# Performance work log

Hardware: AMD Instinct MI355X
Metric: run time of the kernel (lower is better)

Reference implementation:

```python
import jax, jax.numpy as jnp
import numpy as np

ITERATION = 10

def setup_inputs() -> dict:
    key = jax.random.key(0)
    k1, k2, k3 = jax.random.split(key, 3)
    a_inter = jax.random.normal(k1, (8, 64, 64, 32, 32), dtype=jnp.float32)
    logits = jax.random.normal(k2, (8, 64), dtype=jnp.float32)
    W = jax.random.normal(k3, (1, 64, 64), dtype=jnp.float32)
    return {"a_inter": a_inter, "logits": logits, "W": W}


def reference(a_inter, logits, W):
    N = W.shape[1]  # num_nodes
    B = a_inter.shape[0]
    # feats: [B, N, C*H*W]
    feats = a_inter[:, :, :N, :, :].reshape(B, N, -1)
    # expand logits [B, N] -> [B, N, N] (unsqueeze(1).expand in torch)
    logits0 = jnp.broadcast_to(logits[:, None, :], (B, N, N))

    feats_norm = jnp.linalg.norm(feats, ord=2, axis=2, keepdims=True)  # [B, N, 1]
    pairwise_norm = feats_norm @ jnp.swapaxes(feats_norm, 1, 2)        # [B, N, N]
    pairwise_dot = feats @ jnp.swapaxes(feats, 1, 2)                   # [B, N, N]
    pairwise_sim = pairwise_dot / (pairwise_norm + 1e-6)
    W_sym = (W + jnp.swapaxes(W, 1, 2)) / 2.0
    pairwise_potential = pairwise_sim * W_sym                          # [B, N, N]

    unary_potential = logits0

    def body(i, l):
        probs = jnp.swapaxes(jax.nn.sigmoid(l), 1, 2)  # [B, N, N]
        # probs*pp - (1-probs)*pp == (2*probs - 1)*pp
        pp_E = jnp.sum((2.0 * probs - 1.0) * pairwise_potential, axis=2, keepdims=True)
        return unary_potential + pp_E

    logits_out = jax.lax.fori_loop(0, ITERATION, body, logits0)
    return logits_out.mean(axis=1)  # [B, N]
```

## Files before the change

### kernel.cpp

```cpp
#include <hip/hip_runtime.h>
#include <math.h>

#define BATCH 8
#define NN 64
#define DD 65536
#define CH 128
#define KC (DD / CH)
#define BK 64
#define NIT (KC / BK)
#define LSTRIDE 72

typedef float  floatx4 __attribute__((ext_vector_type(4)));
typedef __bf16 bf16x8  __attribute__((ext_vector_type(8)));

static __device__ __forceinline__ unsigned short f2bf(float f) {
    union { float f; unsigned u; } x;
    x.f = f;
    unsigned r = x.u + 0x7FFFu + ((x.u >> 16) & 1u);
    return (unsigned short)(r >> 16);
}

__global__ __launch_bounds__(256) void gram_partial_kernel(const float* __restrict__ a,
                                                           float* __restrict__ part) {
    __shared__ __align__(16) unsigned short lds[2][NN * LSTRIDE];

    const int bid = blockIdx.x;
    const int b = bid >> 7;
    const int c = bid & (CH - 1);
    const float* base = a + (size_t)b * NN * DD + (size_t)c * KC;

    const int tid  = threadIdx.x;
    const int w    = tid >> 6;
    const int lane = tid & 63;
    const int m    = lane & 15;
    const int q    = lane >> 4;

    int rowv[4], kqv[4];
    for (int sub = 0; sub < 4; ++sub) {
        int F = sub * 256 + tid;
        rowv[sub] = F >> 4;
        kqv[sub]  = F & 15;
    }

    floatx4 acc[4];
    for (int t = 0; t < 4; ++t) acc[t] = (floatx4)0.0f;

    float4 regs[4];
    for (int sub = 0; sub < 4; ++sub)
        regs[sub] = *(const float4*)(base + (size_t)rowv[sub] * DD + kqv[sub] * 4);

    for (int kt = 0; kt < NIT; ++kt) {
        unsigned short* buf = lds[kt & 1];

        for (int sub = 0; sub < 4; ++sub) {
            ushort4 h;
            h.x = f2bf(regs[sub].x);
            h.y = f2bf(regs[sub].y);
            h.z = f2bf(regs[sub].z);
            h.w = f2bf(regs[sub].w);
            *reinterpret_cast<ushort4*>(&buf[rowv[sub] * LSTRIDE + kqv[sub] * 4]) = h;
        }
        __syncthreads();

        if (kt + 1 < NIT) {
            const float* nb = base + (size_t)(kt + 1) * BK;
            for (int sub = 0; sub < 4; ++sub)
                regs[sub] = *(const float4*)(nb + (size_t)rowv[sub] * DD + kqv[sub] * 4);
        }

        for (int s = 0; s < 2; ++s) {
            int kb = s * 32 + q * 8;
            bf16x8 fr[4];
            for (int t = 0; t < 4; ++t)
                fr[t] = *reinterpret_cast<const bf16x8*>(&buf[(16 * t + m) * LSTRIDE + kb]);
            bf16x8 A = fr[w];
            for (int t = 0; t < 4; ++t)
                acc[t] = __builtin_amdgcn_mfma_f32_16x16x32_bf16(A, fr[t], acc[t], 0, 0, 0);
        }
    }

    float* pg = part + (size_t)bid * (NN * NN);
    for (int t = 0; t < 4; ++t)
        for (int r = 0; r < 4; ++r) {
            int i = 16 * w + q * 4 + r;
            int j = 16 * t + m;
            pg[i * NN + j] = acc[t][r];
        }
}

__global__ __launch_bounds__(128) void gram_reduce_kernel(const float* __restrict__ part,
                                                          float* __restrict__ gram) {
    const int gid = blockIdx.x * 128 + threadIdx.x;
    const int b   = gid >> 12;
    const int idx = gid & 4095;
    const float* p = part + (size_t)b * CH * (NN * NN) + idx;

    float s0 = 0.f, s1 = 0.f, s2 = 0.f, s3 = 0.f;
    #pragma unroll
    for (int c = 0; c < CH; c += 4) {
        s0 += p[(size_t)(c + 0) * (NN * NN)];
        s1 += p[(size_t)(c + 1) * (NN * NN)];
        s2 += p[(size_t)(c + 2) * (NN * NN)];
        s3 += p[(size_t)(c + 3) * (NN * NN)];
    }
    gram[gid] = (s0 + s1) + (s2 + s3);
}

__global__ __launch_bounds__(256) void crf_kernel(const float* __restrict__ gram,
                                                  const float* __restrict__ logits,
                                                  const float* __restrict__ Wm,
                                                  float* __restrict__ out) {
    __shared__ float pp[NN][NN + 1];
    __shared__ float E[NN];
    __shared__ float nrm[NN];
    __shared__ float part[4 * NN];

    const int b  = blockIdx.x;
    const int tid = threadIdx.x;
    const int i  = tid & 63;
    const int jq = tid >> 6;
    const float* g = gram + b * NN * NN;

    if (jq == 0) nrm[i] = sqrtf(g[i * NN + i]);
    E[i] = 0.0f;
    __syncthreads();

    const float ni = nrm[i];
    for (int jj = 0; jj < 16; ++jj) {
        int j = jq * 16 + jj;
        float wsym = 0.5f * (Wm[i * NN + j] + Wm[j * NN + i]);
        pp[i][j] = g[i * NN + j] / (ni * nrm[j] + 1e-6f) * wsym;
    }
    const float li = logits[b * NN + i];
    __syncthreads();

    for (int it = 0; it < 10; ++it) {
        float acc = 0.0f;
        for (int jj = 0; jj < 16; ++jj) {
            int j = jq * 16 + jj;
            float t = li + E[j];
            float s = 1.0f / (1.0f + expf(-t));
            acc = fmaf(2.0f * s - 1.0f, pp[i][j], acc);
        }
        part[jq * NN + i] = acc;
        __syncthreads();
        if (jq == 0)
            E[i] = part[i] + part[NN + i] + part[2 * NN + i] + part[3 * NN + i];
        __syncthreads();
    }

    if (tid < 64) {
        float s = E[tid];
        for (int off = 32; off > 0; off >>= 1) s += __shfl_down(s, off);
        float meanE = __shfl(s, 0) * (1.0f / 64.0f);
        out[b * NN + tid] = logits[b * NN + tid] + meanE;
    }
}

extern "C" void kernel_launch(void* const* d_in, const int* in_sizes, int n_in,
                              void* d_out, int out_size, void* d_ws, size_t ws_size,
                              hipStream_t stream) {
    const float* a      = (const float*)d_in[0];
    const float* logits = (const float*)d_in[1];
    const float* Wm     = (const float*)d_in[2];
    float* out  = (float*)d_out;

    float* part = (float*)d_ws;
    float* gram = part + (size_t)BATCH * CH * NN * NN;

    gram_partial_kernel<<<BATCH * CH, 256, 0, stream>>>(a, part);
    gram_reduce_kernel<<<(BATCH * NN * NN) / 128, 128, 0, stream>>>(part, gram);
    crf_kernel<<<BATCH, 256, 0, stream>>>(gram, logits, Wm, out);
}
```

Before: 261.2 us.

## Load MFMA fragments directly from global memory, dropping LDS staging

The gram partial kernel stops staging bf16 tiles through shared memory. Each lane now loads its MFMA fragments straight from global memory, converts them by truncation with a byte-permute instead of round-to-nearest, and unrolls the whole K loop without barriers. The partial output is written in a tiled 16x16 layout, and the reduce kernel's indexing is adjusted to match. This removes the LDS round trip and the __syncthreads calls. In exchange, each row is loaded redundantly by all four waves and bf16 truncation adds rounding bias.

```diff
diff --git a/kernel.cpp b/kernel.cpp
--- a/kernel.cpp
+++ b/kernel.cpp
@@ -6,28 +6,26 @@
 #define DD 65536
 #define CH 128
 #define KC (DD / CH)
-#define BK 64
-#define NIT (KC / BK)
-#define LSTRIDE 72
+#define KSTEPS (KC / 32)
 
 typedef float  floatx4 __attribute__((ext_vector_type(4)));
 typedef __bf16 bf16x8  __attribute__((ext_vector_type(8)));
 
-static __device__ __forceinline__ unsigned short f2bf(float f) {
-    union { float f; unsigned u; } x;
-    x.f = f;
-    unsigned r = x.u + 0x7FFFu + ((x.u >> 16) & 1u);
-    return (unsigned short)(r >> 16);
+static __device__ __forceinline__ bf16x8 cvt8(float4 lo, float4 hi) {
+    const unsigned sel = 0x07060302u;
+    union { unsigned u[4]; bf16x8 v; } r;
+    r.u[0] = __builtin_amdgcn_perm(__float_as_uint(lo.y), __float_as_uint(lo.x), sel);
+    r.u[1] = __builtin_amdgcn_perm(__float_as_uint(lo.w), __float_as_uint(lo.z), sel);
+    r.u[2] = __builtin_amdgcn_perm(__float_as_uint(hi.y), __float_as_uint(hi.x), sel);
+    r.u[3] = __builtin_amdgcn_perm(__float_as_uint(hi.w), __float_as_uint(hi.z), sel);
+    return r.v;
 }
 
-__global__ __launch_bounds__(256) void gram_partial_kernel(const float* __restrict__ a,
-                                                           float* __restrict__ part) {
-    __shared__ __align__(16) unsigned short lds[2][NN * LSTRIDE];
-
+__global__ __launch_bounds__(256, 4) void gram_partial_kernel(const float* __restrict__ a,
+                                                              float* __restrict__ part) {
     const int bid = blockIdx.x;
     const int b = bid >> 7;
     const int c = bid & (CH - 1);
-    const float* base = a + (size_t)b * NN * DD + (size_t)c * KC;
 
     const int tid  = threadIdx.x;
     const int w    = tid >> 6;
@@ -35,57 +33,49 @@
     const int m    = lane & 15;
     const int q    = lane >> 4;
 
-    int rowv[4], kqv[4];
-    for (int sub = 0; sub < 4; ++sub) {
-        int F = sub * 256 + tid;
-        rowv[sub] = F >> 4;
-        kqv[sub]  = F & 15;
-    }
+    const float* base = a + (size_t)b * NN * DD + (size_t)c * KC
+                          + (size_t)m * DD + q * 8;
+    const float* p[4];
+    #pragma unroll
+    for (int i = 0; i < 4; ++i)
+        p[i] = base + (size_t)((w ^ i) * 16) * DD;
 
     floatx4 acc[4];
-    for (int t = 0; t < 4; ++t) acc[t] = (floatx4)0.0f;
+    #pragma unroll
+    for (int i = 0; i < 4; ++i) acc[i] = (floatx4)0.0f;
 
-    float4 regs[4];
-    for (int sub = 0; sub < 4; ++sub)
-        regs[sub] = *(const float4*)(base + (size_t)rowv[sub] * DD + kqv[sub] * 4);
+    #pragma unroll
+    for (int s = 0; s < KSTEPS; ++s) {
+        const int o = s * 32;
+        float4 l0 = *(const float4*)(p[0] + o);
+        float4 h0 = *(const float4*)(p[0] + o + 4);
+        float4 l1 = *(const float4*)(p[1] + o);
+        float4 h1 = *(const float4*)(p[1] + o + 4);
+        float4 l2 = *(const float4*)(p[2] + o);
+        float4 h2 = *(const float4*)(p[2] + o + 4);
+        float4 l3 = *(const float4*)(p[3] + o);
+        float4 h3 = *(const float4*)(p[3] + o + 4);
 
-    for (int kt = 0; kt < NIT; ++kt) {
-        unsigned short* buf = lds[kt & 1];
+        bf16x8 f0 = cvt8(l0, h0);
+        bf16x8 f1 = cvt8(l1, h1);
+        bf16x8 f2 = cvt8(l2, h2);
+        bf16x8 f3 = cvt8(l3, h3);
 
-        for (int sub = 0; sub < 4; ++sub) {
-            ushort4 h;
-            h.x = f2bf(regs[sub].x);
-            h.y = f2bf(regs[sub].y);
-            h.z = f2bf(regs[sub].z);
-            h.w = f2bf(regs[sub].w);
-            *reinterpret_cast<ushort4*>(&buf[rowv[sub] * LSTRIDE + kqv[sub] * 4]) = h;
-        }
-        __syncthreads();
-
-        if (kt + 1 < NIT) {
-            const float* nb = base + (size_t)(kt + 1) * BK;
-            for (int sub = 0; sub < 4; ++sub)
-                regs[sub] = *(const float4*)(nb + (size_t)rowv[sub] * DD + kqv[sub] * 4);
-        }
-
-        for (int s = 0; s < 2; ++s) {
-            int kb = s * 32 + q * 8;
-            bf16x8 fr[4];
-            for (int t = 0; t < 4; ++t)
-                fr[t] = *reinterpret_cast<const bf16x8*>(&buf[(16 * t + m) * LSTRIDE + kb]);
-            bf16x8 A = fr[w];
-            for (int t = 0; t < 4; ++t)
-                acc[t] = __builtin_amdgcn_mfma_f32_16x16x32_bf16(A, fr[t], acc[t], 0, 0, 0);
-        }
+        acc[0] = __builtin_amdgcn_mfma_f32_16x16x32_bf16(f0, f0, acc[0], 0, 0, 0);
+        acc[1] = __builtin_amdgcn_mfma_f32_16x16x32_bf16(f0, f1, acc[1], 0, 0, 0);
+        acc[2] = __builtin_amdgcn_mfma_f32_16x16x32_bf16(f0, f2, acc[2], 0, 0, 0);
+        acc[3] = __builtin_amdgcn_mfma_f32_16x16x32_bf16(f0, f3, acc[3], 0, 0, 0);
     }
 
     float* pg = part + (size_t)bid * (NN * NN);
-    for (int t = 0; t < 4; ++t)
-        for (int r = 0; r < 4; ++r) {
-            int i = 16 * w + q * 4 + r;
-            int j = 16 * t + m;
-            pg[i * NN + j] = acc[t][r];
-        }
+    #pragma unroll
+    for (int i = 0; i < 4; ++i) {
+        const int t = w ^ i;
+        float* tp = pg + (w * 4 + t) * 256 + m;
+        #pragma unroll
+        for (int r = 0; r < 4; ++r)
+            tp[(q * 4 + r) * 16] = acc[i][r];
+    }
 }
 
 __global__ __launch_bounds__(128) void gram_reduce_kernel(const float* __restrict__ part,
@@ -93,7 +83,10 @@
     const int gid = blockIdx.x * 128 + threadIdx.x;
     const int b   = gid >> 12;
     const int idx = gid & 4095;
-    const float* p = part + (size_t)b * CH * (NN * NN) + idx;
+    const int i   = idx >> 6;
+    const int j   = idx & 63;
+    const int off = ((i >> 4) * 4 + (j >> 4)) * 256 + (i & 15) * 16 + (j & 15);
+    const float* p = part + (size_t)b * CH * (NN * NN) + off;
 
     float s0 = 0.f, s1 = 0.f, s2 = 0.f, s3 = 0.f;
     #pragma unroll
```

Result: faster. 236.4 us (-9.5%).
